# Optimization experiments

Hardware: AMD Instinct MI355X
Metric: run time of the kernel (lower is better)

The kernel has to match this reference:

```python
import jax, jax.numpy as jnp
import numpy as np

N = 100000
E = 800000
HID = 128
HEADS = 4
NEG_SLOPE = 0.2


def _mlp2(x, w1, b1, w2, b2):
    h = jax.nn.relu(x @ w1.T + b1)
    return jax.nn.relu(h @ w2.T + b2)


def gat_conv(h, src, dst, lin_w, att_src, att_dst, bias, heads, out_ch, concat):
    # h: [N, in] -> hl: [N, heads, out_ch]
    n = h.shape[0]
    hl = (h @ lin_w.T).reshape(n, heads, out_ch)
    a_s = jnp.sum(hl * att_src, axis=-1)  # [N, heads]
    a_d = jnp.sum(hl * att_dst, axis=-1)
    alpha = jax.nn.leaky_relu(a_s[src] + a_d[dst], NEG_SLOPE)  # [E', heads]
    amax = jax.ops.segment_max(alpha, dst, num_segments=n)
    ex = jnp.exp(alpha - amax[dst])
    denom = jax.ops.segment_sum(ex, dst, num_segments=n)
    att = ex / denom[dst]  # segment softmax over incoming edges
    msg = hl[src] * att[:, :, None]  # [E', heads, out_ch]
    out = jax.ops.segment_sum(msg, dst, num_segments=n)
    out = out.reshape(n, heads * out_ch) if concat else out.mean(axis=1)
    return out + bias


def setup_inputs() -> dict:
    key = jax.random.key(0)
    ks = iter(jax.random.split(key, 40))
    g = lambda shape: (jax.random.normal(next(ks), shape, dtype=jnp.float32) * 0.1)
    inp = {}
    inp['x'] = jax.random.normal(next(ks), (N, 2), dtype=jnp.float32)
    inp['node_types'] = jax.random.randint(next(ks), (N,), 0, 2, dtype=jnp.int32)
    inp['edge_index'] = jax.random.randint(next(ks), (2, E), 0, N, dtype=jnp.int64)
    # heterogeneous encoder
    inp['ew1'] = g((HID, 2)); inp['eb1'] = g((HID,))
    inp['ew2'] = g((HID, HID)); inp['eb2'] = g((HID,))
    inp['cw1'] = g((HID, 1)); inp['cb1'] = g((HID,))
    inp['cw2'] = g((HID, HID)); inp['cb2'] = g((HID,))
    # GAT layers 0,1: heads=4, out_ch=HID//4, concat
    C = HID // HEADS
    inp['lin0'] = g((HID, HID)); inp['as0'] = g((HEADS, C)); inp['ad0'] = g((HEADS, C)); inp['b0'] = g((HID,))
    inp['lin1'] = g((HID, HID)); inp['as1'] = g((HEADS, C)); inp['ad1'] = g((HEADS, C)); inp['b1'] = g((HID,))
    # GAT layer 2: heads=1, out_ch=HID, concat=False
    inp['lin2'] = g((HID, HID)); inp['as2'] = g((1, HID)); inp['ad2'] = g((1, HID)); inp['b2'] = g((HID,))
    # decoder
    inp['dw1'] = g((HID, HID)); inp['db1'] = g((HID,))
    inp['dw2'] = g((HID // 2, HID)); inp['db2'] = g((HID // 2,))
    inp['dw3'] = g((1, HID // 2)); inp['db3'] = g((1,))
    return inp


def reference(x, node_types, edge_index, ew1, eb1, ew2, eb2, cw1, cb1, cw2, cb2,
              lin0, as0, ad0, b0, lin1, as1, ad1, b1, lin2, as2, ad2, b2,
              dw1, db1, dw2, db2, dw3, db3):
    n = x.shape[0]
    # heterogeneous encoding (vectorized type select)
    item_h = _mlp2(x[:, :2], ew1, eb1, ew2, eb2)
    con_h = _mlp2(x[:, :1], cw1, cb1, cw2, cb2)
    item_mask = node_types == 0
    h = jnp.where(item_mask[:, None], item_h, jnp.where((node_types == 1)[:, None], con_h, 0.0))
    # add self-loops (PyG GATConv default add_self_loops=True)
    loop = jnp.arange(n, dtype=edge_index.dtype)
    src = jnp.concatenate([edge_index[0], loop])
    dst = jnp.concatenate([edge_index[1], loop])
    C = HID // HEADS
    h0 = jax.nn.relu(gat_conv(h, src, dst, lin0, as0, ad0, b0, HEADS, C, True))
    h1 = h0 + jax.nn.relu(gat_conv(h0, src, dst, lin1, as1, ad1, b1, HEADS, C, True))
    h2 = h1 + jax.nn.relu(gat_conv(h1, src, dst, lin2, as2, ad2, b2, 1, HID, False))
    # decoder on all nodes; zero out non-item nodes (dropout is eval/no-op)
    d = jax.nn.relu(h2 @ dw1.T + db1)
    d = jax.nn.relu(d @ dw2.T + db2)
    probs = jax.nn.sigmoid(d @ dw3.T + db3).squeeze(-1)
    return probs * item_mask.astype(probs.dtype)
```

## Files before the change

### kernel.cpp

```cpp
#include <hip/hip_runtime.h>
#include <math.h>

#define HIDDEN 128
#define NEG_SLOPE 0.2f

typedef unsigned short u16;
typedef __attribute__((ext_vector_type(8))) short bf16x8;
typedef __attribute__((ext_vector_type(4))) float f32x4;

__device__ __forceinline__ u16 f2bf(float f) {
    unsigned u = __float_as_uint(f);
    unsigned r = (u + 0x7FFFu + ((u >> 16) & 1u)) >> 16;
    return (u16)r;
}
__device__ __forceinline__ float bf2f(u16 u) {
    return __uint_as_float((unsigned)u << 16);
}
__device__ __forceinline__ unsigned pack2(float a, float b) {
    return (unsigned)f2bf(a) | ((unsigned)f2bf(b) << 16);
}
__device__ __forceinline__ float lo16f(unsigned v) { return bf2f((u16)v); }
__device__ __forceinline__ float hi16f(unsigned v) { return bf2f((u16)(v >> 16)); }

struct WPtrs { const float* p[7]; };
__global__ void convw_kernel(WPtrs wp, unsigned* __restrict__ wb, int totalPairs) {
    int i = blockIdx.x * blockDim.x + threadIdx.x;
    if (i >= totalPairs) return;
    int e = i * 2;
    int seg, off;
    if (e < 98304) { seg = e >> 14; off = e & 16383; }
    else           { seg = 6;       off = e - 98304; }
    const float* s = wp.p[seg];
    wb[i] = pack2(s[off], s[off + 1]);
}

template <int OUT, int DH>
__global__ __launch_bounds__(256) void gemm_mfma_kernel(
        const u16* __restrict__ X, const u16* __restrict__ Wb,
        const float* __restrict__ bias, const int* __restrict__ types,
        u16* __restrict__ out, float* __restrict__ a_s, float* __restrict__ a_d,
        const float* __restrict__ att_s, const float* __restrict__ att_d,
        const float* __restrict__ dw3, const float* __restrict__ db3,
        float* __restrict__ fout, int N, int mode) {
    constexpr int NT = OUT / 16;
    __shared__ u16 Xs[64 * 136];
    __shared__ u16 Ws[OUT * 136];
    const int tid = threadIdx.x;
    const int n0 = blockIdx.x * 64;

#pragma unroll
    for (int r = 0; r < 4; r++) {
        int j = r * 256 + tid;
        int row = j >> 4, c8 = (j & 15) << 3;
        int n = n0 + row;
        uint4 v = make_uint4(0u, 0u, 0u, 0u);
        if (n < N) v = *(const uint4*)&X[(size_t)n * 128 + c8];
        *(uint4*)&Xs[row * 136 + c8] = v;
    }
#pragma unroll
    for (int r = 0; r < NT; r++) {
        int j = r * 256 + tid;
        int row = j >> 4, c8 = (j & 15) << 3;
        *(uint4*)&Ws[row * 136 + c8] = *(const uint4*)&Wb[(size_t)row * 128 + c8];
    }
    __syncthreads();

    const int w = tid >> 6, lane = tid & 63;
    const int qd = lane >> 4, lr = lane & 15;

    f32x4 acc[NT];
#pragma unroll
    for (int j = 0; j < NT; j++) acc[j] = (f32x4){0.f, 0.f, 0.f, 0.f};

#pragma unroll
    for (int k = 0; k < 4; k++) {
        bf16x8 a = *(const bf16x8*)&Xs[(w * 16 + lr) * 136 + k * 32 + qd * 8];
#pragma unroll
        for (int j = 0; j < NT; j++) {
            bf16x8 b = *(const bf16x8*)&Ws[(j * 16 + lr) * 136 + k * 32 + qd * 8];
            acc[j] = __builtin_amdgcn_mfma_f32_16x16x32_bf16(a, b, acc[j], 0, 0, 0);
        }
    }

    if (mode == 3) {
        float pr[4] = {0.f, 0.f, 0.f, 0.f};
#pragma unroll
        for (int j = 0; j < NT; j++) {
            int col = j * 16 + lr;
            float b = bias[col], wv = dw3[col];
#pragma unroll
            for (int r = 0; r < 4; r++) pr[r] += fmaxf(acc[j][r] + b, 0.f) * wv;
        }
#pragma unroll
        for (int m = 1; m < 16; m <<= 1)
#pragma unroll
            for (int r = 0; r < 4; r++) pr[r] += __shfl_xor(pr[r], m, 64);
        if (lr == 0) {
            float b3 = db3[0];
#pragma unroll
            for (int r = 0; r < 4; r++) {
                int row = n0 + w * 16 + qd * 4 + r;
                if (row < N) {
                    float prob = 1.f / (1.f + expf(-(pr[r] + b3)));
                    fout[row] = (types[row] == 0) ? prob : 0.f;
                }
            }
        }
        return;
    }

    if (DH > 0) {
        constexpr int NH = (DH == 4) ? 4 : 1;
        float sp[NH][4], dp[NH][4];
#pragma unroll
        for (int h = 0; h < NH; h++)
#pragma unroll
            for (int r = 0; r < 4; r++) { sp[h][r] = 0.f; dp[h][r] = 0.f; }
#pragma unroll
        for (int j = 0; j < NT; j++) {
            int col = j * 16 + lr;
            float as_ = att_s[col], ad_ = att_d[col];
            int h = (DH == 4) ? (j >> 1) : 0;
#pragma unroll
            for (int r = 0; r < 4; r++) {
                sp[h][r] += acc[j][r] * as_;
                dp[h][r] += acc[j][r] * ad_;
            }
        }
#pragma unroll
        for (int m = 1; m < 16; m <<= 1)
#pragma unroll
            for (int h = 0; h < NH; h++)
#pragma unroll
                for (int r = 0; r < 4; r++) {
                    sp[h][r] += __shfl_xor(sp[h][r], m, 64);
                    dp[h][r] += __shfl_xor(dp[h][r], m, 64);
                }
        if (lr == 0) {
#pragma unroll
            for (int r = 0; r < 4; r++) {
                int row = n0 + w * 16 + qd * 4 + r;
                if (row < N) {
#pragma unroll
                    for (int h = 0; h < NH; h++) {
                        a_s[row * DH + h] = sp[h][r];
                        a_d[row * DH + h] = dp[h][r];
                    }
                }
            }
        }
    }

#pragma unroll
    for (int r = 0; r < 4; r++) {
        int row = n0 + w * 16 + qd * 4 + r;
        if (row >= N) continue;
        int ty = (mode == 2) ? types[row] : 0;
        if (mode == 2 && ty == 0) continue;
#pragma unroll
        for (int j = 0; j < NT; j++) {
            int col = j * 16 + lr;
            float v = acc[j][r];
            if (mode >= 1) v = fmaxf(v + bias[col], 0.f);
            if (mode == 2 && ty != 1) v = 0.f;
            out[(size_t)row * OUT + col] = f2bf(v);
        }
    }
}

__global__ void enc_h1_kernel(const float* __restrict__ x,
                              const float* __restrict__ ew1, const float* __restrict__ eb1,
                              const float* __restrict__ cw1, const float* __restrict__ cb1,
                              u16* __restrict__ h1_item, u16* __restrict__ h1_con, int N) {
    int i = blockIdx.x * blockDim.x + threadIdx.x;
    if (i >= N * 64) return;
    int n = i >> 6, t = (i & 63) * 2;
    float x0 = x[2 * n], x1 = x[2 * n + 1];
    float i0 = fmaxf(ew1[2 * t] * x0 + ew1[2 * t + 1] * x1 + eb1[t], 0.f);
    float i1 = fmaxf(ew1[2 * t + 2] * x0 + ew1[2 * t + 3] * x1 + eb1[t + 1], 0.f);
    float c0 = fmaxf(cw1[t] * x0 + cb1[t], 0.f);
    float c1 = fmaxf(cw1[t + 1] * x0 + cb1[t + 1], 0.f);
    *(unsigned*)&h1_item[(size_t)n * 128 + t] = pack2(i0, i1);
    *(unsigned*)&h1_con[(size_t)n * 128 + t]  = pack2(c0, c1);
}

__global__ void zero1_kernel(int* __restrict__ a, int N) {
    int i = blockIdx.x * blockDim.x + threadIdx.x;
    if (i < N) a[i] = 0;
}

__global__ void hist_kernel(const int* __restrict__ ei, int E, int E2,
                            int* __restrict__ cnt, int* __restrict__ pos) {
    int e = blockIdx.x * blockDim.x + threadIdx.x;
    if (e >= E2) return;
    int d = (e < E) ? ei[E + e] : e - E;
    pos[e] = atomicAdd(&cnt[d], 1);
}

__global__ void scan1_kernel(const int* __restrict__ cnt, int* __restrict__ rs,
                             int* __restrict__ bsum, int N) {
    __shared__ int s[256];
    int i = blockIdx.x * 256 + threadIdx.x;
    int v = (i < N) ? cnt[i] : 0;
    s[threadIdx.x] = v;
    __syncthreads();
    for (int off = 1; off < 256; off <<= 1) {
        int t = (threadIdx.x >= off) ? s[threadIdx.x - off] : 0;
        __syncthreads();
        s[threadIdx.x] += t;
        __syncthreads();
    }
    if (i < N) rs[i] = s[threadIdx.x];
    if (threadIdx.x == 255) bsum[blockIdx.x] = s[255];
}

__global__ void scan2_kernel(int* __restrict__ bsum, int nb) {
    __shared__ int s[1024];
    int i = threadIdx.x;
    int v = (i < nb) ? bsum[i] : 0;
    s[i] = v;
    __syncthreads();
    for (int off = 1; off < 1024; off <<= 1) {
        int t = (i >= off) ? s[i - off] : 0;
        __syncthreads();
        s[i] += t;
        __syncthreads();
    }
    if (i < nb) bsum[i] = s[i] - v;
}

__global__ void scan3_kernel(int* __restrict__ rs, const int* __restrict__ cnt,
                             const int* __restrict__ bsum, int N) {
    int i = blockIdx.x * 256 + threadIdx.x;
    if (i < N) rs[i] = rs[i] - cnt[i] + bsum[blockIdx.x];
}

__global__ void scatter_kernel(const int* __restrict__ ei, int E, int E2,
                               const int* __restrict__ rs, const int* __restrict__ pos,
                               int* __restrict__ srclist) {
    int e = blockIdx.x * blockDim.x + threadIdx.x;
    if (e >= E2) return;
    int s, d;
    if (e < E) { s = ei[e]; d = ei[E + e]; }
    else       { s = d = e - E; }
    srclist[rs[d] + pos[e]] = s;
}

template <int H>
__global__ void att_kernel(const int* __restrict__ rs, const int* __restrict__ cnt,
                           const int* __restrict__ srclist,
                           const float* __restrict__ a_s, const float* __restrict__ a_d,
                           float* __restrict__ ex, float* __restrict__ dinv, int N) {
    int i = blockIdx.x * blockDim.x + threadIdx.x;
    if (i >= N * H) return;
    int n = (H == 1) ? i : (i >> 2);
    int h = (H == 1) ? 0 : (i & 3);
    int beg = rs[n], deg = cnt[n];
    float ad = a_d[i];
    float l = 0.f;
    for (int k = 0; k < deg; k++) {
        float al = a_s[srclist[beg + k] * H + h] + ad;
        al = (al > 0.f) ? al : NEG_SLOPE * al;
        float p = expf(fminf(al, 80.f));
        ex[(beg + k) * H + h] = p;
        l += p;
    }
    dinv[i] = 1.f / l;
}

template <int H>
__global__ __launch_bounds__(256) void gat_agg_kernel(
        const int* __restrict__ rs, const int* __restrict__ cnt,
        const int* __restrict__ srclist, const u16* __restrict__ hl,
        const float* __restrict__ ex, const float* __restrict__ dinv,
        const float* __restrict__ bias, const u16* __restrict__ res,
        u16* __restrict__ out, int N) {
    int n = blockIdx.x * 4 + (threadIdx.x >> 6);
    int l = threadIdx.x & 63;
    if (n >= N) return;
    const int g = l >> 4;
    const int c = l & 15;
    const int head = (H == 1) ? 0 : (c >> 2);
    const int beg = rs[n];
    const int deg = cnt[n];
    float acc0[8], acc1[8];
#pragma unroll
    for (int j = 0; j < 8; j++) { acc0[j] = 0.f; acc1[j] = 0.f; }

    for (int k = 0; k < deg; k += 8) {
        int i0 = k + g;
        int i1 = k + 4 + g;
        int e0 = beg + min(i0, deg - 1);
        int e1 = beg + min(i1, deg - 1);
        int s0 = srclist[e0];
        int s1 = srclist[e1];
        float p0 = ex[e0 * H + head];
        float p1 = ex[e1 * H + head];
        if (i0 >= deg) p0 = 0.f;
        if (i1 >= deg) p1 = 0.f;
        uint4 v0 = *(const uint4*)&hl[(size_t)s0 * 128 + 8 * c];
        uint4 v1 = *(const uint4*)&hl[(size_t)s1 * 128 + 8 * c];
        acc0[0] += p0 * lo16f(v0.x); acc0[1] += p0 * hi16f(v0.x);
        acc0[2] += p0 * lo16f(v0.y); acc0[3] += p0 * hi16f(v0.y);
        acc0[4] += p0 * lo16f(v0.z); acc0[5] += p0 * hi16f(v0.z);
        acc0[6] += p0 * lo16f(v0.w); acc0[7] += p0 * hi16f(v0.w);
        acc1[0] += p1 * lo16f(v1.x); acc1[1] += p1 * hi16f(v1.x);
        acc1[2] += p1 * lo16f(v1.y); acc1[3] += p1 * hi16f(v1.y);
        acc1[4] += p1 * lo16f(v1.z); acc1[5] += p1 * hi16f(v1.z);
        acc1[6] += p1 * lo16f(v1.w); acc1[7] += p1 * hi16f(v1.w);
    }
#pragma unroll
    for (int j = 0; j < 8; j++) {
        float a = acc0[j] + acc1[j];
        a += __shfl_xor(a, 16, 64);
        a += __shfl_xor(a, 32, 64);
        acc0[j] = a;
    }
    if (g == 0) {
        float di = dinv[n * H + head];
        float4 b0 = *(const float4*)&bias[8 * c];
        float4 b1 = *(const float4*)&bias[8 * c + 4];
        float o[8];
        o[0] = fmaxf(acc0[0] * di + b0.x, 0.f);
        o[1] = fmaxf(acc0[1] * di + b0.y, 0.f);
        o[2] = fmaxf(acc0[2] * di + b0.z, 0.f);
        o[3] = fmaxf(acc0[3] * di + b0.w, 0.f);
        o[4] = fmaxf(acc0[4] * di + b1.x, 0.f);
        o[5] = fmaxf(acc0[5] * di + b1.y, 0.f);
        o[6] = fmaxf(acc0[6] * di + b1.z, 0.f);
        o[7] = fmaxf(acc0[7] * di + b1.w, 0.f);
        if (res) {
            uint4 rv = *(const uint4*)&res[(size_t)n * 128 + 8 * c];
            o[0] += lo16f(rv.x); o[1] += hi16f(rv.x);
            o[2] += lo16f(rv.y); o[3] += hi16f(rv.y);
            o[4] += lo16f(rv.z); o[5] += hi16f(rv.z);
            o[6] += lo16f(rv.w); o[7] += hi16f(rv.w);
        }
        uint4 ov = make_uint4(pack2(o[0], o[1]), pack2(o[2], o[3]),
                              pack2(o[4], o[5]), pack2(o[6], o[7]));
        *(uint4*)&out[(size_t)n * 128 + 8 * c] = ov;
    }
}

template <int H>
static void gat_layer(const u16* X, const u16* lin, const float* as_, const float* ad_,
                      const float* bias, const u16* res, u16* hl, u16* outb,
                      float* a_s, float* a_d, float* ex, float* dinv,
                      const int* rs, const int* cnt, const int* srclist,
                      int N, hipStream_t stream) {
    int gx = (N + 63) / 64;
    gemm_mfma_kernel<128, H><<<gx, 256, 0, stream>>>(
        X, lin, nullptr, nullptr, hl, a_s, a_d, as_, ad_, nullptr, nullptr, nullptr, N, 0);
    att_kernel<H><<<(N * H + 255) / 256, 256, 0, stream>>>(rs, cnt, srclist, a_s, a_d,
                                                           ex, dinv, N);
    gat_agg_kernel<H><<<(N + 3) / 4, 256, 0, stream>>>(rs, cnt, srclist, hl, ex, dinv,
                                                       bias, res, outb, N);
}

extern "C" void kernel_launch(void* const* d_in, const int* in_sizes, int n_in,
                              void* d_out, int out_size, void* d_ws, size_t ws_size,
                              hipStream_t stream) {
    const float* x     = (const float*)d_in[0];
    const int*   types = (const int*)d_in[1];
    const int*   ei    = (const int*)d_in[2];
    const float* ew1 = (const float*)d_in[3];
    const float* eb1 = (const float*)d_in[4];
    const float* ew2 = (const float*)d_in[5];
    const float* eb2 = (const float*)d_in[6];
    const float* cw1 = (const float*)d_in[7];
    const float* cb1 = (const float*)d_in[8];
    const float* cw2 = (const float*)d_in[9];
    const float* cb2 = (const float*)d_in[10];
    const float* lin0 = (const float*)d_in[11];
    const float* as0  = (const float*)d_in[12];
    const float* ad0  = (const float*)d_in[13];
    const float* b0   = (const float*)d_in[14];
    const float* lin1 = (const float*)d_in[15];
    const float* as1  = (const float*)d_in[16];
    const float* ad1  = (const float*)d_in[17];
    const float* b1   = (const float*)d_in[18];
    const float* lin2 = (const float*)d_in[19];
    const float* as2  = (const float*)d_in[20];
    const float* ad2  = (const float*)d_in[21];
    const float* b2   = (const float*)d_in[22];
    const float* dw1 = (const float*)d_in[23];
    const float* db1 = (const float*)d_in[24];
    const float* dw2 = (const float*)d_in[25];
    const float* db2 = (const float*)d_in[26];
    const float* dw3 = (const float*)d_in[27];
    const float* db3 = (const float*)d_in[28];

    int N  = in_sizes[1];
    int E  = in_sizes[2] / 2;
    int E2 = E + N;

    size_t NF = (size_t)N * HIDDEN;
    u16* bufA = (u16*)d_ws;
    u16* bufB = bufA + NF;
    u16* bufC = bufB + NF;
    float* fbase = (float*)(bufC + NF);
    float* a_s  = fbase;
    float* a_d  = a_s + (size_t)N * 4;
    float* dinv = a_d + (size_t)N * 4;
    float* ex   = dinv + (size_t)N * 4;
    int* rs      = (int*)(ex + (size_t)E2 * 4);
    int* cnt     = rs + N;
    int* pos     = cnt + N;
    int* bsum    = pos + E2;
    int* srclist = bsum + 1024;
    u16* wb      = (u16*)(srclist + E2);
    u16* wb_ew2  = wb;
    u16* wb_cw2  = wb + 16384;
    u16* wb_lin0 = wb + 32768;
    u16* wb_lin1 = wb + 49152;
    u16* wb_lin2 = wb + 65536;
    u16* wb_dw1  = wb + 81920;
    u16* wb_dw2  = wb + 98304;

    int nb = (N + 255) / 256;

    WPtrs wp;
    wp.p[0] = ew2; wp.p[1] = cw2; wp.p[2] = lin0; wp.p[3] = lin1;
    wp.p[4] = lin2; wp.p[5] = dw1; wp.p[6] = dw2;
    convw_kernel<<<(53248 + 255) / 256, 256, 0, stream>>>(wp, (unsigned*)wb, 53248);

    zero1_kernel<<<nb, 256, 0, stream>>>(cnt, N);
    hist_kernel<<<(E2 + 255) / 256, 256, 0, stream>>>(ei, E, E2, cnt, pos);
    scan1_kernel<<<nb, 256, 0, stream>>>(cnt, rs, bsum, N);
    scan2_kernel<<<1, 1024, 0, stream>>>(bsum, nb);
    scan3_kernel<<<nb, 256, 0, stream>>>(rs, cnt, bsum, N);
    scatter_kernel<<<(E2 + 255) / 256, 256, 0, stream>>>(ei, E, E2, rs, pos, srclist);

    int gx = (N + 63) / 64;

    enc_h1_kernel<<<(N * 64 + 255) / 256, 256, 0, stream>>>(x, ew1, eb1, cw1, cb1,
                                                            bufB, bufC, N);
    gemm_mfma_kernel<128, 0><<<gx, 256, 0, stream>>>(
        bufB, wb_ew2, eb2, nullptr, bufA, nullptr, nullptr, nullptr, nullptr,
        nullptr, nullptr, nullptr, N, 1);
    gemm_mfma_kernel<128, 0><<<gx, 256, 0, stream>>>(
        bufC, wb_cw2, cb2, types, bufA, nullptr, nullptr, nullptr, nullptr,
        nullptr, nullptr, nullptr, N, 2);

    gat_layer<4>(bufA, wb_lin0, as0, ad0, b0, nullptr, bufB, bufA,
                 a_s, a_d, ex, dinv, rs, cnt, srclist, N, stream);
    gat_layer<4>(bufA, wb_lin1, as1, ad1, b1, bufA, bufB, bufC,
                 a_s, a_d, ex, dinv, rs, cnt, srclist, N, stream);
    gat_layer<1>(bufC, wb_lin2, as2, ad2, b2, bufC, bufB, bufA,
                 a_s, a_d, ex, dinv, rs, cnt, srclist, N, stream);

    gemm_mfma_kernel<128, 0><<<gx, 256, 0, stream>>>(
        bufA, wb_dw1, db1, nullptr, bufC, nullptr, nullptr, nullptr, nullptr,
        nullptr, nullptr, nullptr, N, 1);
    gemm_mfma_kernel<64, 0><<<gx, 256, 0, stream>>>(
        bufC, wb_dw2, db2, types, nullptr, nullptr, nullptr, nullptr, nullptr,
        dw3, db3, (float*)d_out, N, 3);
}
```

Before: 550.6 us.

## Fuse encoder MLPs into one kernel, merge scan and zero kernels, unroll aggregation

Replaces the separate first-layer encoder kernel and two GEMM launches with a single encoder kernel. It computes both layer-1 activations directly into shared memory, runs both MFMA GEMMs, and selects the output per node type. This avoids writing and reading two N×128 bf16 intermediates and cuts launches. The zero-count kernel is folded into weight conversion, and scan2/scan3 are merged so each block sums its own prefix. The GAT aggregation loop now processes 12 edges per iteration instead of 8, for more memory-level parallelism at the cost of more registers.

```diff
diff --git a/kernel.cpp b/kernel.cpp
--- a/kernel.cpp
+++ b/kernel.cpp
@@ -23,15 +23,117 @@
 __device__ __forceinline__ float hi16f(unsigned v) { return bf2f((u16)(v >> 16)); }
 
 struct WPtrs { const float* p[7]; };
-__global__ void convw_kernel(WPtrs wp, unsigned* __restrict__ wb, int totalPairs) {
+__global__ void convw_zero_kernel(WPtrs wp, unsigned* __restrict__ wb, int totalPairs,
+                                  int* __restrict__ cnt, int N) {
     int i = blockIdx.x * blockDim.x + threadIdx.x;
-    if (i >= totalPairs) return;
-    int e = i * 2;
-    int seg, off;
-    if (e < 98304) { seg = e >> 14; off = e & 16383; }
-    else           { seg = 6;       off = e - 98304; }
-    const float* s = wp.p[seg];
-    wb[i] = pack2(s[off], s[off + 1]);
+    if (i < N) cnt[i] = 0;
+    if (i < totalPairs) {
+        int e = i * 2;
+        int seg, off;
+        if (e < 98304) { seg = e >> 14; off = e & 16383; }
+        else           { seg = 6;       off = e - 98304; }
+        const float* s = wp.p[seg];
+        wb[i] = pack2(s[off], s[off + 1]);
+    }
+}
+
+__global__ __launch_bounds__(256) void encoder_kernel(
+        const float* __restrict__ x, const int* __restrict__ types,
+        const float* __restrict__ ew1, const float* __restrict__ eb1,
+        const float* __restrict__ cw1, const float* __restrict__ cb1,
+        const u16* __restrict__ wb_ew2, const u16* __restrict__ wb_cw2,
+        const float* __restrict__ eb2, const float* __restrict__ cb2,
+        u16* __restrict__ out, int N) {
+    __shared__ u16 Xs[64 * 136];
+    __shared__ u16 Ws[128 * 136];
+    __shared__ float xsh[128];
+    __shared__ float w1sh[640];
+    const int tid = threadIdx.x;
+    const int n0 = blockIdx.x * 64;
+
+    if (tid < 128) {
+        int n = n0 + (tid >> 1);
+        xsh[tid] = (n < N) ? x[2 * n + (tid & 1)] : 0.f;
+    }
+    if (tid < 256) w1sh[tid] = ew1[tid];
+    if (tid < 128) { w1sh[256 + tid] = eb1[tid]; w1sh[384 + tid] = cw1[tid];
+                     w1sh[512 + tid] = cb1[tid]; }
+    __syncthreads();
+
+#pragma unroll
+    for (int r = 0; r < 32; r++) {
+        int j = tid + 256 * r;
+        int row = j >> 7, t = j & 127;
+        float v = fmaxf(w1sh[2 * t] * xsh[2 * row] + w1sh[2 * t + 1] * xsh[2 * row + 1]
+                        + w1sh[256 + t], 0.f);
+        Xs[row * 136 + t] = f2bf(v);
+    }
+#pragma unroll
+    for (int r = 0; r < 8; r++) {
+        int j = r * 256 + tid;
+        int row = j >> 4, c8 = (j & 15) << 3;
+        *(uint4*)&Ws[row * 136 + c8] = *(const uint4*)&wb_ew2[(size_t)row * 128 + c8];
+    }
+    __syncthreads();
+
+    const int w = tid >> 6, lane = tid & 63;
+    const int qd = lane >> 4, lr = lane & 15;
+
+    f32x4 acc_i[8], acc_c[8];
+#pragma unroll
+    for (int j = 0; j < 8; j++) acc_i[j] = (f32x4){0.f, 0.f, 0.f, 0.f};
+#pragma unroll
+    for (int k = 0; k < 4; k++) {
+        bf16x8 a = *(const bf16x8*)&Xs[(w * 16 + lr) * 136 + k * 32 + qd * 8];
+#pragma unroll
+        for (int j = 0; j < 8; j++) {
+            bf16x8 b = *(const bf16x8*)&Ws[(j * 16 + lr) * 136 + k * 32 + qd * 8];
+            acc_i[j] = __builtin_amdgcn_mfma_f32_16x16x32_bf16(a, b, acc_i[j], 0, 0, 0);
+        }
+    }
+    __syncthreads();
+
+#pragma unroll
+    for (int r = 0; r < 32; r++) {
+        int j = tid + 256 * r;
+        int row = j >> 7, t = j & 127;
+        float v = fmaxf(w1sh[384 + t] * xsh[2 * row] + w1sh[512 + t], 0.f);
+        Xs[row * 136 + t] = f2bf(v);
+    }
+#pragma unroll
+    for (int r = 0; r < 8; r++) {
+        int j = r * 256 + tid;
+        int row = j >> 4, c8 = (j & 15) << 3;
+        *(uint4*)&Ws[row * 136 + c8] = *(const uint4*)&wb_cw2[(size_t)row * 128 + c8];
+    }
+    __syncthreads();
+#pragma unroll
+    for (int j = 0; j < 8; j++) acc_c[j] = (f32x4){0.f, 0.f, 0.f, 0.f};
+#pragma unroll
+    for (int k = 0; k < 4; k++) {
+        bf16x8 a = *(const bf16x8*)&Xs[(w * 16 + lr) * 136 + k * 32 + qd * 8];
+#pragma unroll
+        for (int j = 0; j < 8; j++) {
+            bf16x8 b = *(const bf16x8*)&Ws[(j * 16 + lr) * 136 + k * 32 + qd * 8];
+            acc_c[j] = __builtin_amdgcn_mfma_f32_16x16x32_bf16(a, b, acc_c[j], 0, 0, 0);
+        }
+    }
+
+#pragma unroll
+    for (int r = 0; r < 4; r++) {
+        int row = n0 + w * 16 + qd * 4 + r;
+        if (row >= N) continue;
+        int ty = types[row];
+#pragma unroll
+        for (int j = 0; j < 8; j++) {
+            int col = j * 16 + lr;
+            float v;
+            if (ty == 0)      v = fmaxf(acc_i[j][r] + eb2[col], 0.f);
+            else if (ty == 1) v = fmaxf(acc_c[j][r] + cb2[col], 0.f);
+            else              v = 0.f;
+            out[(size_t)row * HIDDEN + col] = f2bf(v);
+        }
+    }
 }
 
 template <int OUT, int DH>
@@ -155,38 +257,14 @@
     for (int r = 0; r < 4; r++) {
         int row = n0 + w * 16 + qd * 4 + r;
         if (row >= N) continue;
-        int ty = (mode == 2) ? types[row] : 0;
-        if (mode == 2 && ty == 0) continue;
 #pragma unroll
         for (int j = 0; j < NT; j++) {
             int col = j * 16 + lr;
             float v = acc[j][r];
             if (mode >= 1) v = fmaxf(v + bias[col], 0.f);
-            if (mode == 2 && ty != 1) v = 0.f;
             out[(size_t)row * OUT + col] = f2bf(v);
         }
     }
-}
-
-__global__ void enc_h1_kernel(const float* __restrict__ x,
-                              const float* __restrict__ ew1, const float* __restrict__ eb1,
-                              const float* __restrict__ cw1, const float* __restrict__ cb1,
-                              u16* __restrict__ h1_item, u16* __restrict__ h1_con, int N) {
-    int i = blockIdx.x * blockDim.x + threadIdx.x;
-    if (i >= N * 64) return;
-    int n = i >> 6, t = (i & 63) * 2;
-    float x0 = x[2 * n], x1 = x[2 * n + 1];
-    float i0 = fmaxf(ew1[2 * t] * x0 + ew1[2 * t + 1] * x1 + eb1[t], 0.f);
-    float i1 = fmaxf(ew1[2 * t + 2] * x0 + ew1[2 * t + 3] * x1 + eb1[t + 1], 0.f);
-    float c0 = fmaxf(cw1[t] * x0 + cb1[t], 0.f);
-    float c1 = fmaxf(cw1[t + 1] * x0 + cb1[t + 1], 0.f);
-    *(unsigned*)&h1_item[(size_t)n * 128 + t] = pack2(i0, i1);
-    *(unsigned*)&h1_con[(size_t)n * 128 + t]  = pack2(c0, c1);
-}
-
-__global__ void zero1_kernel(int* __restrict__ a, int N) {
-    int i = blockIdx.x * blockDim.x + threadIdx.x;
-    if (i < N) a[i] = 0;
 }
 
 __global__ void hist_kernel(const int* __restrict__ ei, int E, int E2,
@@ -214,25 +292,21 @@
     if (threadIdx.x == 255) bsum[blockIdx.x] = s[255];
 }
 
-__global__ void scan2_kernel(int* __restrict__ bsum, int nb) {
-    __shared__ int s[1024];
-    int i = threadIdx.x;
-    int v = (i < nb) ? bsum[i] : 0;
-    s[i] = v;
-    __syncthreads();
-    for (int off = 1; off < 1024; off <<= 1) {
-        int t = (i >= off) ? s[i - off] : 0;
+__global__ void scan23_kernel(int* __restrict__ rs, const int* __restrict__ cnt,
+                              const int* __restrict__ bsum, int N) {
+    __shared__ int sdata[256];
+    int b = blockIdx.x;
+    int partial = 0;
+    for (int i = threadIdx.x; i < b; i += 256) partial += bsum[i];
+    sdata[threadIdx.x] = partial;
+    __syncthreads();
+    for (int off = 128; off; off >>= 1) {
+        if (threadIdx.x < off) sdata[threadIdx.x] += sdata[threadIdx.x + off];
         __syncthreads();
-        s[i] += t;
-        __syncthreads();
-    }
-    if (i < nb) bsum[i] = s[i] - v;
-}
-
-__global__ void scan3_kernel(int* __restrict__ rs, const int* __restrict__ cnt,
-                             const int* __restrict__ bsum, int N) {
-    int i = blockIdx.x * 256 + threadIdx.x;
-    if (i < N) rs[i] = rs[i] - cnt[i] + bsum[blockIdx.x];
+    }
+    int pre = sdata[0];
+    int i = b * 256 + threadIdx.x;
+    if (i < N) rs[i] = rs[i] - cnt[i] + pre;
 }
 
 __global__ void scatter_kernel(const int* __restrict__ ei, int E, int E2,
@@ -283,23 +357,25 @@
     const int head = (H == 1) ? 0 : (c >> 2);
     const int beg = rs[n];
     const int deg = cnt[n];
-    float acc0[8], acc1[8];
-#pragma unroll
-    for (int j = 0; j < 8; j++) { acc0[j] = 0.f; acc1[j] = 0.f; }
-
-    for (int k = 0; k < deg; k += 8) {
-        int i0 = k + g;
-        int i1 = k + 4 + g;
+    float acc0[8], acc1[8], acc2[8];
+#pragma unroll
+    for (int j = 0; j < 8; j++) { acc0[j] = 0.f; acc1[j] = 0.f; acc2[j] = 0.f; }
+
+    for (int k = 0; k < deg; k += 12) {
+        int i0 = k + g, i1 = k + 4 + g, i2 = k + 8 + g;
         int e0 = beg + min(i0, deg - 1);
         int e1 = beg + min(i1, deg - 1);
-        int s0 = srclist[e0];
-        int s1 = srclist[e1];
+        int e2 = beg + min(i2, deg - 1);
+        int s0 = srclist[e0], s1 = srclist[e1], s2 = srclist[e2];
         float p0 = ex[e0 * H + head];
         float p1 = ex[e1 * H + head];
+        float p2 = ex[e2 * H + head];
         if (i0 >= deg) p0 = 0.f;
         if (i1 >= deg) p1 = 0.f;
+        if (i2 >= deg) p2 = 0.f;
         uint4 v0 = *(const uint4*)&hl[(size_t)s0 * 128 + 8 * c];
         uint4 v1 = *(const uint4*)&hl[(size_t)s1 * 128 + 8 * c];
+        uint4 v2 = *(const uint4*)&hl[(size_t)s2 * 128 + 8 * c];
         acc0[0] += p0 * lo16f(v0.x); acc0[1] += p0 * hi16f(v0.x);
         acc0[2] += p0 * lo16f(v0.y); acc0[3] += p0 * hi16f(v0.y);
         acc0[4] += p0 * lo16f(v0.z); acc0[5] += p0 * hi16f(v0.z);
@@ -308,10 +384,14 @@
         acc1[2] += p1 * lo16f(v1.y); acc1[3] += p1 * hi16f(v1.y);
         acc1[4] += p1 * lo16f(v1.z); acc1[5] += p1 * hi16f(v1.z);
         acc1[6] += p1 * lo16f(v1.w); acc1[7] += p1 * hi16f(v1.w);
+        acc2[0] += p2 * lo16f(v2.x); acc2[1] += p2 * hi16f(v2.x);
+        acc2[2] += p2 * lo16f(v2.y); acc2[3] += p2 * hi16f(v2.y);
+        acc2[4] += p2 * lo16f(v2.z); acc2[5] += p2 * hi16f(v2.z);
+        acc2[6] += p2 * lo16f(v2.w); acc2[7] += p2 * hi16f(v2.w);
     }
 #pragma unroll
     for (int j = 0; j < 8; j++) {
-        float a = acc0[j] + acc1[j];
+        float a = acc0[j] + acc1[j] + acc2[j];
         a += __shfl_xor(a, 16, 64);
         a += __shfl_xor(a, 32, 64);
         acc0[j] = a;
@@ -422,25 +502,19 @@
     WPtrs wp;
     wp.p[0] = ew2; wp.p[1] = cw2; wp.p[2] = lin0; wp.p[3] = lin1;
     wp.p[4] = lin2; wp.p[5] = dw1; wp.p[6] = dw2;
-    convw_kernel<<<(53248 + 255) / 256, 256, 0, stream>>>(wp, (unsigned*)wb, 53248);
-
-    zero1_kernel<<<nb, 256, 0, stream>>>(cnt, N);
+    int cz = max(N, 53248);
+    convw_zero_kernel<<<(cz + 255) / 256, 256, 0, stream>>>(wp, (unsigned*)wb, 53248,
+                                                            cnt, N);
+
     hist_kernel<<<(E2 + 255) / 256, 256, 0, stream>>>(ei, E, E2, cnt, pos);
     scan1_kernel<<<nb, 256, 0, stream>>>(cnt, rs, bsum, N);
-    scan2_kernel<<<1, 1024, 0, stream>>>(bsum, nb);
-    scan3_kernel<<<nb, 256, 0, stream>>>(rs, cnt, bsum, N);
+    scan23_kernel<<<nb, 256, 0, stream>>>(rs, cnt, bsum, N);
     scatter_kernel<<<(E2 + 255) / 256, 256, 0, stream>>>(ei, E, E2, rs, pos, srclist);
 
     int gx = (N + 63) / 64;
 
-    enc_h1_kernel<<<(N * 64 + 255) / 256, 256, 0, stream>>>(x, ew1, eb1, cw1, cb1,
-                                                            bufB, bufC, N);
-    gemm_mfma_kernel<128, 0><<<gx, 256, 0, stream>>>(
-        bufB, wb_ew2, eb2, nullptr, bufA, nullptr, nullptr, nullptr, nullptr,
-        nullptr, nullptr, nullptr, N, 1);
-    gemm_mfma_kernel<128, 0><<<gx, 256, 0, stream>>>(
-        bufC, wb_cw2, cb2, types, bufA, nullptr, nullptr, nullptr, nullptr,
-        nullptr, nullptr, nullptr, N, 2);
+    encoder_kernel<<<gx, 256, 0, stream>>>(x, types, ew1, eb1, cw1, cb1,
+                                           wb_ew2, wb_cw2, eb2, cb2, bufA, N);
 
     gat_layer<4>(bufA, wb_lin0, as0, ad0, b0, nullptr, bufB, bufA,
                  a_s, a_d, ex, dinv, rs, cnt, srclist, N, stream);
```

After: 512.5 us. -6.9%, faster.
